# Optimization experiments

Measured on AMD Instinct MI355X. Metric: run time of the kernel, lower is better.

The kernel has to match this reference:

```python
import jax, jax.numpy as jnp
import numpy as np

DECAY = 0.99
EPS = 1e-05


def setup_inputs() -> dict:
    key = jax.random.key(0)
    k1, k2 = jax.random.split(key)
    N, D, K = 262144, 32, 1024
    z = jax.random.normal(k1, (N, D), dtype=jnp.float32)
    # xavier_normal_ on (K, D): std = sqrt(2 / (K + D))
    std = float(np.sqrt(2.0 / (K + D)))
    embedding = jax.random.normal(k2, (K, D), dtype=jnp.float32) * std
    embed_avg = embedding  # buffer initialized as a clone of the codebook
    cluster_size = jnp.ones((K,), dtype=jnp.float32)
    return {"z": z, "embedding": embedding, "embed_avg": embed_avg,
            "cluster_size": cluster_size}


def reference(z, embedding, embed_avg, cluster_size):
    n_embed, embed_dim = embedding.shape
    # squared euclidean cdist: ||z||^2 + ||e||^2 - 2 z e^T  -> [N, K]
    d = (jnp.sum(z * z, axis=1, keepdims=True)
         + jnp.sum(embedding * embedding, axis=1)
         - 2.0 * (z @ embedding.T))
    encoding_indices = jnp.argmin(d, axis=1)  # [N]
    # one-hot column sums via scatter-add (counts per code)
    counts = jnp.zeros((n_embed,), z.dtype).at[encoding_indices].add(1.0)
    unused_codes = jnp.sum(counts == 0)
    # embedding gather
    z_q = embedding[encoding_indices]  # [N, D]
    # EMA scatter-add update (training branch, use_ema=True)
    embed_sum = jnp.zeros_like(embedding).at[encoding_indices].add(z)  # [K, D]
    cluster_size_new = DECAY * cluster_size + (1.0 - DECAY) * counts
    embed_avg_new = DECAY * embed_avg + (1.0 - DECAY) * embed_sum
    n = jnp.sum(cluster_size_new)
    norm_w = n * (cluster_size_new + EPS) / (n + n_embed * EPS)  # Laplace smoothing
    embedding_new = embed_avg_new / norm_w[:, None]
    codebook_loss = jnp.float32(0.0)
    commitment_loss = jnp.mean((z - jax.lax.stop_gradient(z_q)) ** 2)
    # straight-through estimator
    z_q_out = z + jax.lax.stop_gradient(z_q - z)
    return (z_q_out, codebook_loss, commitment_loss, encoding_indices,
            unused_codes, embedding_new, cluster_size_new, embed_avg_new)
```

## Files before the change

kernel.cpp:

```cpp
#include <hip/hip_runtime.h>
#include <hip/hip_bf16.h>
#include <float.h>

#define DIM 32
#define KCODES 1024
#define NROWS 262144

#define O_ZQ   0
#define O_CB   8388608
#define O_CL   8388609
#define O_IDX  8388610
#define O_UN   8650754
#define O_EMB  8650755
#define O_CS   8683523
#define O_EA   8684547

#define W_PCNT 0
#define W_PSUM 262144
#define W_PCOM 8650752
#define W_NORM 8651008
#define W_ZZH  8652032
#define W_EEH  8914176
#define W_BF   8915200

typedef __attribute__((ext_vector_type(8))) short bf16x8;
typedef __attribute__((ext_vector_type(4))) float f32x4;

#define MFMA16 __builtin_amdgcn_mfma_f32_16x16x32_bf16

static __device__ __forceinline__ unsigned short f2bf(float x) {
    __hip_bfloat16 h = __float2bfloat16(x);
    return __builtin_bit_cast(unsigned short, h);
}
static __device__ __forceinline__ float bf2f(unsigned short u) {
    unsigned int v = ((unsigned int)u) << 16;
    return __builtin_bit_cast(float, v);
}
static __device__ __forceinline__ float pw8_sq(const float* x) {
    float w[32];
    #pragma unroll
    for (int i = 0; i < 32; ++i) w[i] = __fmul_rn(x[i], x[i]);
    float r[8];
    #pragma unroll
    for (int j = 0; j < 8; ++j) r[j] = ((w[j] + w[8 + j]) + w[16 + j]) + w[24 + j];
    return ((r[0] + r[1]) + (r[2] + r[3])) + ((r[4] + r[5]) + (r[6] + r[7]));
}

__global__ __launch_bounds__(256) void vq_prep_z(
    const float* __restrict__ z, float* __restrict__ ws)
{
    int row = blockIdx.x * 256 + threadIdx.x;
    float x[32];
    const float4* zg = (const float4*)(z + (size_t)row * DIM);
    #pragma unroll
    for (int q = 0; q < 8; ++q) {
        float4 v = zg[q];
        x[4*q] = v.x; x[4*q+1] = v.y; x[4*q+2] = v.z; x[4*q+3] = v.w;
    }
    ws[W_ZZH + row] = 0.5f * pw8_sq(x);
}

__global__ __launch_bounds__(256) void vq_prep_e(
    const float* __restrict__ emb, float* __restrict__ ws)
{
    int c = blockIdx.x * 256 + threadIdx.x;
    float x[32];
    const float4* eg = (const float4*)(emb + (size_t)c * DIM);
    #pragma unroll
    for (int q = 0; q < 8; ++q) {
        float4 v = eg[q];
        x[4*q] = v.x; x[4*q+1] = v.y; x[4*q+2] = v.z; x[4*q+3] = v.w;
    }
    ws[W_EEH + c] = 0.5f * pw8_sq(x);

    unsigned short hb[3][32];
    #pragma unroll
    for (int i = 0; i < 32; ++i) {
        float v = x[i];
        unsigned short h0 = f2bf(v); float f0 = bf2f(h0); float r1 = v - f0;
        unsigned short h1 = f2bf(r1); float f1 = bf2f(h1); float r2 = r1 - f1;
        unsigned short h2 = f2bf(r2);
        hb[0][i] = h0; hb[1][i] = h1; hb[2][i] = h2;
    }
    bf16x8* bf = (bf16x8*)(ws + W_BF);
    int kt = c >> 4, cl = c & 15;
    #pragma unroll
    for (int s = 0; s < 3; ++s) {
        #pragma unroll
        for (int j = 0; j < 4; ++j) {
            bf16x8 pk;
            #pragma unroll
            for (int e = 0; e < 8; ++e) pk[e] = (short)hb[s][j*8 + e];
            bf[(kt*3 + s)*64 + j*16 + cl] = pk;
        }
    }
}

__global__ __launch_bounds__(256, 4) void vq_argmin_mfma(
    const float* __restrict__ z, const float* __restrict__ wsc,
    float* __restrict__ out)
{
    __shared__ float eesh[1024];
    const int t = threadIdx.x;
    const int lane = t & 63, w = t >> 6;
    const int g = lane >> 4, lr = lane & 15;

    const bf16x8* bvG = (const bf16x8*)(wsc + W_BF);

    #pragma unroll
    for (int i = 0; i < 4; ++i) eesh[t + i * 256] = wsc[W_EEH + t + i * 256];

    const int rtbase = blockIdx.x * 16 + w * 4;
    bf16x8 zh[4], zm[4], zl[4];
    float zza[4][4];
    #pragma unroll
    for (int j = 0; j < 4; ++j) {
        const int rtg = rtbase + j;
        const float* zp = z + ((size_t)(rtg * 16 + lr)) * DIM + g * 8;
        float4 a4 = *(const float4*)zp, b4 = *(const float4*)(zp + 4);
        float xs[8] = {a4.x, a4.y, a4.z, a4.w, b4.x, b4.y, b4.z, b4.w};
        #pragma unroll
        for (int e = 0; e < 8; ++e) {
            float v = xs[e];
            unsigned short h0 = f2bf(v); float f0 = bf2f(h0); float r1 = v - f0;
            unsigned short h1 = f2bf(r1); float f1 = bf2f(h1); float r2 = r1 - f1;
            zh[j][e] = (short)h0; zm[j][e] = (short)h1; zl[j][e] = (short)f2bf(r2);
        }
        float4 zv = *(const float4*)(wsc + W_ZZH + rtg * 16 + g * 4);
        zza[j][0] = zv.x; zza[j][1] = zv.y; zza[j][2] = zv.z; zza[j][3] = zv.w;
    }

    unsigned int Bb[4][4]; int Kk[4][4];
    #pragma unroll
    for (int j = 0; j < 4; ++j)
        #pragma unroll
        for (int r = 0; r < 4; ++r) { Bb[j][r] = 0xFFFFFFFFu; Kk[j][r] = 0; }

    __syncthreads();

    #pragma unroll 2
    for (int kt = 0; kt < 64; ++kt) {
        bf16x8 eh = bvG[(kt * 3 + 0) * 64 + lane];
        bf16x8 em = bvG[(kt * 3 + 1) * 64 + lane];
        bf16x8 el = bvG[(kt * 3 + 2) * 64 + lane];
        float ee_l = eesh[kt * 16 + lr];
        int kge = kt * 16 + lr;
        #pragma unroll
        for (int j = 0; j < 4; ++j) {
            f32x4 a = {0.f, 0.f, 0.f, 0.f};
            a = MFMA16(zh[j], eh, a, 0, 0, 0);
            a = MFMA16(zh[j], em, a, 0, 0, 0);
            a = MFMA16(zm[j], eh, a, 0, 0, 0);
            a = MFMA16(zh[j], el, a, 0, 0, 0);
            a = MFMA16(zl[j], eh, a, 0, 0, 0);
            a = MFMA16(zm[j], em, a, 0, 0, 0);
            #pragma unroll
            for (int r = 0; r < 4; ++r) {
                float v = (zza[j][r] + ee_l) - a[r];
                unsigned int u = __builtin_bit_cast(unsigned int, v);
                bool tk = u < Bb[j][r];
                Bb[j][r] = tk ? u : Bb[j][r];
                Kk[j][r] = tk ? kge : Kk[j][r];
            }
        }
    }

    #pragma unroll
    for (int j = 0; j < 4; ++j) {
        const int rtg = rtbase + j;
        #pragma unroll
        for (int r = 0; r < 4; ++r) {
            unsigned int b0 = Bb[j][r]; int k0 = Kk[j][r];
            #pragma unroll
            for (int m = 1; m < 16; m <<= 1) {
                unsigned int ob = __shfl_xor((int)b0, m, 16); int ok = __shfl_xor(k0, m, 16);
                bool tk = (ob < b0) || (ob == b0 && ok < k0);
                b0 = tk ? ob : b0; k0 = tk ? ok : k0;
            }
            if (lr == 0) out[O_IDX + rtg * 16 + g * 4 + r] = (float)k0;
        }
    }
}

__global__ __launch_bounds__(1024) void vq_scatter(
    const float* __restrict__ z, const float* __restrict__ emb,
    float* __restrict__ out, float* __restrict__ ws)
{
    __shared__ float smem[34816];
    __shared__ float red[16];
    const int t = threadIdx.x;
    const int b = blockIdx.x;
    {
        float4 zero4 = {0.f, 0.f, 0.f, 0.f};
        float4* s4 = (float4*)smem;
        #pragma unroll
        for (int i = 0; i < 9; ++i) { int j = t + i * 1024; if (j < 8704) s4[j] = zero4; }
    }
    __syncthreads();

    const int row = b * 1024 + t;
    const int kk = (int)out[O_IDX + row];
    const float4* zg = (const float4*)(z + (size_t)row * DIM);
    const float4* eg = (const float4*)(emb + (size_t)kk * DIM);
    float4* og = (float4*)(out + O_ZQ + (size_t)row * DIM);
    float zv[32];
    float csum = 0.f;
    #pragma unroll
    for (int q = 0; q < 8; ++q) {
        float4 v = zg[q];
        float4 e = eg[q];
        zv[4*q] = v.x; zv[4*q+1] = v.y; zv[4*q+2] = v.z; zv[4*q+3] = v.w;
        float d0 = v.x - e.x, d1 = v.y - e.y, d2 = v.z - e.z, d3 = v.w - e.w;
        csum = fmaf(d0, d0, csum); csum = fmaf(d1, d1, csum);
        csum = fmaf(d2, d2, csum); csum = fmaf(d3, d3, csum);
        float4 o;
        o.x = v.x + (e.x - v.x); o.y = v.y + (e.y - v.y);
        o.z = v.z + (e.z - v.z); o.w = v.w + (e.w - v.w);
        og[q] = o;
    }
    atomicAdd(&smem[33792 + kk], 1.0f);
    #pragma unroll
    for (int i = 0; i < 32; ++i) atomicAdd(&smem[kk * 33 + i], zv[i]);

    #pragma unroll
    for (int off = 32; off > 0; off >>= 1) csum += __shfl_down(csum, off, 64);
    if ((t & 63) == 0) red[t >> 6] = csum;
    __syncthreads();

    float cpart = smem[33792 + t];
    if (cpart != 0.f) atomicAdd(&ws[W_PCNT + t], cpart);

    float4* p4 = (float4*)(ws + W_PSUM + (size_t)b * (KCODES * DIM));
    #pragma unroll
    for (int c = 0; c < 8; ++c) {
        int j = t + c * 1024;
        int kr = j >> 3, e0 = (j & 7) * 4;
        float4 v;
        v.x = smem[kr * 33 + e0 + 0]; v.y = smem[kr * 33 + e0 + 1];
        v.z = smem[kr * 33 + e0 + 2]; v.w = smem[kr * 33 + e0 + 3];
        p4[j] = v;
    }
    if (t == 0) {
        float s = 0.f;
        #pragma unroll
        for (int i = 0; i < 16; ++i) s += red[i];
        ws[W_PCOM + b] = s;
    }
}

__global__ __launch_bounds__(1024) void vq_epilogue0(
    const float* __restrict__ cs_in, const float* __restrict__ ws,
    float* __restrict__ out, float* __restrict__ wsw)
{
    __shared__ float s1[1024], s2[1024];
    const int k = threadIdx.x;
    float c = ws[W_PCNT + k];
    float csn = 0.99f * cs_in[k] + 0.01f * c;
    out[O_CS + k] = csn;
    s1[k] = csn;
    s2[k] = (c == 0.f) ? 1.f : 0.f;
    __syncthreads();
    for (int s = 512; s > 0; s >>= 1) {
        if (k < s) { s1[k] += s1[k + s]; s2[k] += s2[k + s]; }
        __syncthreads();
    }
    float n = s1[0];
    float unused = s2[0];
    wsw[W_NORM + k] = n * (csn + 1e-5f) / (n + 1024.f * 1e-5f);
    __syncthreads();
    s1[k] = (k < 256) ? ws[W_PCOM + k] : 0.f;
    __syncthreads();
    for (int s = 512; s > 0; s >>= 1) {
        if (k < s) s1[k] += s1[k + s];
        __syncthreads();
    }
    if (k == 0) {
        out[O_CB] = 0.f;
        out[O_CL] = s1[0] / 8388608.f;
        out[O_UN] = unused;
    }
}

__global__ void vq_epilogue1(
    const float* __restrict__ ea, const float* __restrict__ ws,
    float* __restrict__ out)
{
    const int id = blockIdx.x * 128 + threadIdx.x;
    float es = 0.f;
    for (int bb = 0; bb < 256; ++bb) es += ws[W_PSUM + (size_t)bb * (KCODES * DIM) + id];
    float ean = 0.99f * ea[id] + 0.01f * es;
    out[O_EA + id] = ean;
    out[O_EMB + id] = ean / ws[W_NORM + (id >> 5)];
}

extern "C" void kernel_launch(void* const* d_in, const int* in_sizes, int n_in,
                              void* d_out, int out_size, void* d_ws, size_t ws_size,
                              hipStream_t stream)
{
    const float* z   = (const float*)d_in[0];
    const float* emb = (const float*)d_in[1];
    const float* ea  = (const float*)d_in[2];
    const float* cs  = (const float*)d_in[3];
    float* out = (float*)d_out;
    float* ws  = (float*)d_ws;

    hipMemsetAsync(ws + W_PCNT, 0, KCODES * sizeof(float), stream);
    vq_prep_z<<<1024, 256, 0, stream>>>(z, ws);
    vq_prep_e<<<4, 256, 0, stream>>>(emb, ws);
    vq_argmin_mfma<<<1024, 256, 0, stream>>>(z, ws, out);
    vq_scatter<<<256, 1024, 0, stream>>>(z, emb, out, ws);
    vq_epilogue0<<<1, 1024, 0, stream>>>(cs, ws, out, ws);
    vq_epilogue1<<<256, 128, 0, stream>>>(ea, ws, out);
}
```

Before: 176.8 us.

## Fuse z-norm prep and z_q/commitment output into argmin kernel, halve rows per block

Drops the separate z squared-norm prep kernel and instead computes ||z||^2 inside the argmin kernel with cross-lane shuffles. The straight-through z_q write, the embedding gather and the commitment-loss partial sums also move into the argmin kernel, reconstructing z from its three bf16 splits. Each block now handles 2 row tiles per wave instead of 4, so the grid doubles to 2048 blocks, and the 4-blocks-per-CU launch bound is dropped. This removes one launch and one extra pass over z, and shrinks the scatter kernel to just the atomics. In exchange, each loaded codebook tile is reused over fewer rows, and z values rebuilt from the bf16 splits may differ slightly from the original floats.

```diff
diff --git a/kernel.cpp b/kernel.cpp
--- a/kernel.cpp
+++ b/kernel.cpp
@@ -18,10 +18,9 @@
 #define W_PCNT 0
 #define W_PSUM 262144
 #define W_PCOM 8650752
-#define W_NORM 8651008
-#define W_ZZH  8652032
-#define W_EEH  8914176
-#define W_BF   8915200
+#define W_NORM 8652800
+#define W_EEH  8653824
+#define W_BF   8654848
 
 typedef __attribute__((ext_vector_type(8))) short bf16x8;
 typedef __attribute__((ext_vector_type(4))) float f32x4;
@@ -44,20 +43,6 @@
     #pragma unroll
     for (int j = 0; j < 8; ++j) r[j] = ((w[j] + w[8 + j]) + w[16 + j]) + w[24 + j];
     return ((r[0] + r[1]) + (r[2] + r[3])) + ((r[4] + r[5]) + (r[6] + r[7]));
-}
-
-__global__ __launch_bounds__(256) void vq_prep_z(
-    const float* __restrict__ z, float* __restrict__ ws)
-{
-    int row = blockIdx.x * 256 + threadIdx.x;
-    float x[32];
-    const float4* zg = (const float4*)(z + (size_t)row * DIM);
-    #pragma unroll
-    for (int q = 0; q < 8; ++q) {
-        float4 v = zg[q];
-        x[4*q] = v.x; x[4*q+1] = v.y; x[4*q+2] = v.z; x[4*q+3] = v.w;
-    }
-    ws[W_ZZH + row] = 0.5f * pw8_sq(x);
 }
 
 __global__ __launch_bounds__(256) void vq_prep_e(
@@ -96,11 +81,12 @@
     }
 }
 
-__global__ __launch_bounds__(256, 4) void vq_argmin_mfma(
-    const float* __restrict__ z, const float* __restrict__ wsc,
-    float* __restrict__ out)
+__global__ __launch_bounds__(256) void vq_argmin_mfma(
+    const float* __restrict__ z, const float* __restrict__ emb,
+    const float* __restrict__ wsc, float* __restrict__ out, float* __restrict__ ws)
 {
     __shared__ float eesh[1024];
+    __shared__ float red[4];
     const int t = threadIdx.x;
     const int lane = t & 63, w = t >> 6;
     const int g = lane >> 4, lr = lane & 15;
@@ -110,29 +96,40 @@
     #pragma unroll
     for (int i = 0; i < 4; ++i) eesh[t + i * 256] = wsc[W_EEH + t + i * 256];
 
-    const int rtbase = blockIdx.x * 16 + w * 4;
-    bf16x8 zh[4], zm[4], zl[4];
-    float zza[4][4];
-    #pragma unroll
-    for (int j = 0; j < 4; ++j) {
+    const int rtbase = blockIdx.x * 8 + w * 2;
+    bf16x8 zh[2], zm[2], zl[2];
+    float zza[2][4];
+    #pragma unroll
+    for (int j = 0; j < 2; ++j) {
         const int rtg = rtbase + j;
         const float* zp = z + ((size_t)(rtg * 16 + lr)) * DIM + g * 8;
         float4 a4 = *(const float4*)zp, b4 = *(const float4*)(zp + 4);
         float xs[8] = {a4.x, a4.y, a4.z, a4.w, b4.x, b4.y, b4.z, b4.w};
+        float r8[8];
         #pragma unroll
         for (int e = 0; e < 8; ++e) {
             float v = xs[e];
             unsigned short h0 = f2bf(v); float f0 = bf2f(h0); float r1 = v - f0;
             unsigned short h1 = f2bf(r1); float f1 = bf2f(h1); float r2 = r1 - f1;
             zh[j][e] = (short)h0; zm[j][e] = (short)h1; zl[j][e] = (short)f2bf(r2);
-        }
-        float4 zv = *(const float4*)(wsc + W_ZZH + rtg * 16 + g * 4);
-        zza[j][0] = zv.x; zza[j][1] = zv.y; zza[j][2] = zv.z; zza[j][3] = zv.w;
-    }
-
-    unsigned int Bb[4][4]; int Kk[4][4];
-    #pragma unroll
-    for (int j = 0; j < 4; ++j)
+            float wq = __fmul_rn(v, v);
+            float b16 = __shfl_xor(wq, 16);
+            float b32 = __shfl_xor(wq, 32);
+            float b48 = __shfl_xor(wq, 48);
+            float t1 = (g < 2) ? (wq + b16) : (b32 + b48);
+            float c2 = (g == 0) ? b32 : (g == 1) ? b48 : (g == 2) ? wq : b16;
+            float c3 = (g == 0) ? b48 : (g == 1) ? b32 : (g == 2) ? b16 : wq;
+            r8[e] = (t1 + c2) + c3;
+        }
+        float zzf = ((r8[0] + r8[1]) + (r8[2] + r8[3])) + ((r8[4] + r8[5]) + (r8[6] + r8[7]));
+        float zzh2 = 0.5f * zzf;
+        #pragma unroll
+        for (int r = 0; r < 4; ++r) zza[j][r] = __shfl(zzh2, g * 4 + r, 16);
+    }
+
+    unsigned int Bb[2][4]; int Kk[2][4];
+    #pragma unroll
+    for (int j = 0; j < 2; ++j)
         #pragma unroll
         for (int r = 0; r < 4; ++r) { Bb[j][r] = 0xFFFFFFFFu; Kk[j][r] = 0; }
 
@@ -146,7 +143,7 @@
         float ee_l = eesh[kt * 16 + lr];
         int kge = kt * 16 + lr;
         #pragma unroll
-        for (int j = 0; j < 4; ++j) {
+        for (int j = 0; j < 2; ++j) {
             f32x4 a = {0.f, 0.f, 0.f, 0.f};
             a = MFMA16(zh[j], eh, a, 0, 0, 0);
             a = MFMA16(zh[j], em, a, 0, 0, 0);
@@ -165,9 +162,11 @@
         }
     }
 
-    #pragma unroll
-    for (int j = 0; j < 4; ++j) {
+    float csum = 0.f;
+    #pragma unroll
+    for (int j = 0; j < 2; ++j) {
         const int rtg = rtbase + j;
+        int kfin[4];
         #pragma unroll
         for (int r = 0; r < 4; ++r) {
             unsigned int b0 = Bb[j][r]; int k0 = Kk[j][r];
@@ -177,17 +176,44 @@
                 bool tk = (ob < b0) || (ob == b0 && ok < k0);
                 b0 = tk ? ob : b0; k0 = tk ? ok : k0;
             }
+            kfin[r] = k0;
             if (lr == 0) out[O_IDX + rtg * 16 + g * 4 + r] = (float)k0;
         }
-    }
+        int src = (lr >> 2) * 16;
+        int kr0 = __shfl(kfin[0], src);
+        int kr1 = __shfl(kfin[1], src);
+        int kr2 = __shfl(kfin[2], src);
+        int kr3 = __shfl(kfin[3], src);
+        int sel = lr & 3;
+        int kk = (sel == 0) ? kr0 : (sel == 1) ? kr1 : (sel == 2) ? kr2 : kr3;
+        const float4* ep = (const float4*)(emb + (size_t)kk * DIM + g * 8);
+        float4 e0 = ep[0], e1 = ep[1];
+        float ev[8] = {e0.x, e0.y, e0.z, e0.w, e1.x, e1.y, e1.z, e1.w};
+        float ov[8];
+        #pragma unroll
+        for (int e = 0; e < 8; ++e) {
+            float zv = (bf2f((unsigned short)zh[j][e]) + bf2f((unsigned short)zm[j][e]))
+                     + bf2f((unsigned short)zl[j][e]);
+            float d = zv - ev[e];
+            csum = fmaf(d, d, csum);
+            ov[e] = zv + (ev[e] - zv);
+        }
+        float4* og = (float4*)(out + O_ZQ + (size_t)(rtg * 16 + lr) * DIM + g * 8);
+        og[0] = (float4){ov[0], ov[1], ov[2], ov[3]};
+        og[1] = (float4){ov[4], ov[5], ov[6], ov[7]};
+    }
+    #pragma unroll
+    for (int off = 32; off > 0; off >>= 1) csum += __shfl_down(csum, off, 64);
+    if (lane == 0) red[w] = csum;
+    __syncthreads();
+    if (t == 0) ws[W_PCOM + blockIdx.x] = ((red[0] + red[1]) + (red[2] + red[3]));
 }
 
 __global__ __launch_bounds__(1024) void vq_scatter(
-    const float* __restrict__ z, const float* __restrict__ emb,
-    float* __restrict__ out, float* __restrict__ ws)
+    const float* __restrict__ z, const float* __restrict__ outv,
+    float* __restrict__ ws)
 {
     __shared__ float smem[34816];
-    __shared__ float red[16];
     const int t = threadIdx.x;
     const int b = blockIdx.x;
     {
@@ -199,32 +225,17 @@
     __syncthreads();
 
     const int row = b * 1024 + t;
-    const int kk = (int)out[O_IDX + row];
+    const int kk = (int)outv[O_IDX + row];
     const float4* zg = (const float4*)(z + (size_t)row * DIM);
-    const float4* eg = (const float4*)(emb + (size_t)kk * DIM);
-    float4* og = (float4*)(out + O_ZQ + (size_t)row * DIM);
-    float zv[32];
-    float csum = 0.f;
+    atomicAdd(&smem[33792 + kk], 1.0f);
     #pragma unroll
     for (int q = 0; q < 8; ++q) {
         float4 v = zg[q];
-        float4 e = eg[q];
-        zv[4*q] = v.x; zv[4*q+1] = v.y; zv[4*q+2] = v.z; zv[4*q+3] = v.w;
-        float d0 = v.x - e.x, d1 = v.y - e.y, d2 = v.z - e.z, d3 = v.w - e.w;
-        csum = fmaf(d0, d0, csum); csum = fmaf(d1, d1, csum);
-        csum = fmaf(d2, d2, csum); csum = fmaf(d3, d3, csum);
-        float4 o;
-        o.x = v.x + (e.x - v.x); o.y = v.y + (e.y - v.y);
-        o.z = v.z + (e.z - v.z); o.w = v.w + (e.w - v.w);
-        og[q] = o;
-    }
-    atomicAdd(&smem[33792 + kk], 1.0f);
-    #pragma unroll
-    for (int i = 0; i < 32; ++i) atomicAdd(&smem[kk * 33 + i], zv[i]);
-
-    #pragma unroll
-    for (int off = 32; off > 0; off >>= 1) csum += __shfl_down(csum, off, 64);
-    if ((t & 63) == 0) red[t >> 6] = csum;
+        atomicAdd(&smem[kk * 33 + 4 * q + 0], v.x);
+        atomicAdd(&smem[kk * 33 + 4 * q + 1], v.y);
+        atomicAdd(&smem[kk * 33 + 4 * q + 2], v.z);
+        atomicAdd(&smem[kk * 33 + 4 * q + 3], v.w);
+    }
     __syncthreads();
 
     float cpart = smem[33792 + t];
@@ -240,12 +251,6 @@
         v.z = smem[kr * 33 + e0 + 2]; v.w = smem[kr * 33 + e0 + 3];
         p4[j] = v;
     }
-    if (t == 0) {
-        float s = 0.f;
-        #pragma unroll
-        for (int i = 0; i < 16; ++i) s += red[i];
-        ws[W_PCOM + b] = s;
-    }
 }
 
 __global__ __launch_bounds__(1024) void vq_epilogue0(
@@ -268,7 +273,7 @@
     float unused = s2[0];
     wsw[W_NORM + k] = n * (csn + 1e-5f) / (n + 1024.f * 1e-5f);
     __syncthreads();
-    s1[k] = (k < 256) ? ws[W_PCOM + k] : 0.f;
+    s1[k] = ws[W_PCOM + k] + ws[W_PCOM + 1024 + k];
     __syncthreads();
     for (int s = 512; s > 0; s >>= 1) {
         if (k < s) s1[k] += s1[k + s];
@@ -305,10 +310,9 @@
     float* ws  = (float*)d_ws;
 
     hipMemsetAsync(ws + W_PCNT, 0, KCODES * sizeof(float), stream);
-    vq_prep_z<<<1024, 256, 0, stream>>>(z, ws);
     vq_prep_e<<<4, 256, 0, stream>>>(emb, ws);
-    vq_argmin_mfma<<<1024, 256, 0, stream>>>(z, ws, out);
-    vq_scatter<<<256, 1024, 0, stream>>>(z, emb, out, ws);
+    vq_argmin_mfma<<<2048, 256, 0, stream>>>(z, emb, ws, out, ws);
+    vq_scatter<<<256, 1024, 0, stream>>>(z, out, ws);
     vq_epilogue0<<<1, 1024, 0, stream>>>(cs, ws, out, ws);
     vq_epilogue1<<<256, 128, 0, stream>>>(ea, ws, out);
 }
```

New measurement: 187.3 us. +5.9%, slower.

## Fuse row-norm computation into argmin kernel and halve scatter block count

Applied to the files above, without the earlier changes.

Removes the separate vq_prep_z kernel and computes each row's half squared norm inside the MFMA argmin kernel, combining per-lane partial products with cross-lane shuffles in the same summation order as before. The scatter kernel now handles two rows per thread with 128 blocks instead of 256. That halves the per-block partial-sum buffers that the epilogue has to reduce and cuts the number of partial commitment sums. The aim is to save one kernel launch and one pass over z, plus epilogue reduction traffic, at the cost of lower parallelism in the scatter kernel and extra shuffles in argmin.

```diff
diff --git a/kernel.cpp b/kernel.cpp
--- a/kernel.cpp
+++ b/kernel.cpp
@@ -18,10 +18,9 @@
 #define W_PCNT 0
 #define W_PSUM 262144
 #define W_PCOM 8650752
-#define W_NORM 8651008
-#define W_ZZH  8652032
-#define W_EEH  8914176
-#define W_BF   8915200
+#define W_NORM 8652800
+#define W_EEH  8653824
+#define W_BF   8654848
 
 typedef __attribute__((ext_vector_type(8))) short bf16x8;
 typedef __attribute__((ext_vector_type(4))) float f32x4;
@@ -44,20 +43,6 @@
     #pragma unroll
     for (int j = 0; j < 8; ++j) r[j] = ((w[j] + w[8 + j]) + w[16 + j]) + w[24 + j];
     return ((r[0] + r[1]) + (r[2] + r[3])) + ((r[4] + r[5]) + (r[6] + r[7]));
-}
-
-__global__ __launch_bounds__(256) void vq_prep_z(
-    const float* __restrict__ z, float* __restrict__ ws)
-{
-    int row = blockIdx.x * 256 + threadIdx.x;
-    float x[32];
-    const float4* zg = (const float4*)(z + (size_t)row * DIM);
-    #pragma unroll
-    for (int q = 0; q < 8; ++q) {
-        float4 v = zg[q];
-        x[4*q] = v.x; x[4*q+1] = v.y; x[4*q+2] = v.z; x[4*q+3] = v.w;
-    }
-    ws[W_ZZH + row] = 0.5f * pw8_sq(x);
 }
 
 __global__ __launch_bounds__(256) void vq_prep_e(
@@ -119,15 +104,26 @@
         const float* zp = z + ((size_t)(rtg * 16 + lr)) * DIM + g * 8;
         float4 a4 = *(const float4*)zp, b4 = *(const float4*)(zp + 4);
         float xs[8] = {a4.x, a4.y, a4.z, a4.w, b4.x, b4.y, b4.z, b4.w};
+        float r8[8];
         #pragma unroll
         for (int e = 0; e < 8; ++e) {
             float v = xs[e];
             unsigned short h0 = f2bf(v); float f0 = bf2f(h0); float r1 = v - f0;
             unsigned short h1 = f2bf(r1); float f1 = bf2f(h1); float r2 = r1 - f1;
             zh[j][e] = (short)h0; zm[j][e] = (short)h1; zl[j][e] = (short)f2bf(r2);
-        }
-        float4 zv = *(const float4*)(wsc + W_ZZH + rtg * 16 + g * 4);
-        zza[j][0] = zv.x; zza[j][1] = zv.y; zza[j][2] = zv.z; zza[j][3] = zv.w;
+            float wq = __fmul_rn(v, v);
+            float b16 = __shfl_xor(wq, 16);
+            float b32 = __shfl_xor(wq, 32);
+            float b48 = __shfl_xor(wq, 48);
+            float t1 = (g < 2) ? (wq + b16) : (b32 + b48);
+            float c2 = (g == 0) ? b32 : (g == 1) ? b48 : (g == 2) ? wq : b16;
+            float c3 = (g == 0) ? b48 : (g == 1) ? b32 : (g == 2) ? b16 : wq;
+            r8[e] = (t1 + c2) + c3;
+        }
+        float zzf = ((r8[0] + r8[1]) + (r8[2] + r8[3])) + ((r8[4] + r8[5]) + (r8[6] + r8[7]));
+        float zzh2 = 0.5f * zzf;
+        #pragma unroll
+        for (int r = 0; r < 4; ++r) zza[j][r] = __shfl(zzh2, g * 4 + r, 16);
     }
 
     unsigned int Bb[4][4]; int Kk[4][4];
@@ -198,29 +194,32 @@
     }
     __syncthreads();
 
-    const int row = b * 1024 + t;
-    const int kk = (int)out[O_IDX + row];
-    const float4* zg = (const float4*)(z + (size_t)row * DIM);
-    const float4* eg = (const float4*)(emb + (size_t)kk * DIM);
-    float4* og = (float4*)(out + O_ZQ + (size_t)row * DIM);
-    float zv[32];
     float csum = 0.f;
     #pragma unroll
-    for (int q = 0; q < 8; ++q) {
-        float4 v = zg[q];
-        float4 e = eg[q];
-        zv[4*q] = v.x; zv[4*q+1] = v.y; zv[4*q+2] = v.z; zv[4*q+3] = v.w;
-        float d0 = v.x - e.x, d1 = v.y - e.y, d2 = v.z - e.z, d3 = v.w - e.w;
-        csum = fmaf(d0, d0, csum); csum = fmaf(d1, d1, csum);
-        csum = fmaf(d2, d2, csum); csum = fmaf(d3, d3, csum);
-        float4 o;
-        o.x = v.x + (e.x - v.x); o.y = v.y + (e.y - v.y);
-        o.z = v.z + (e.z - v.z); o.w = v.w + (e.w - v.w);
-        og[q] = o;
-    }
-    atomicAdd(&smem[33792 + kk], 1.0f);
-    #pragma unroll
-    for (int i = 0; i < 32; ++i) atomicAdd(&smem[kk * 33 + i], zv[i]);
+    for (int rr = 0; rr < 2; ++rr) {
+        const int row = b * 2048 + rr * 1024 + t;
+        const int kk = (int)out[O_IDX + row];
+        const float4* zg = (const float4*)(z + (size_t)row * DIM);
+        const float4* eg = (const float4*)(emb + (size_t)kk * DIM);
+        float4* og = (float4*)(out + O_ZQ + (size_t)row * DIM);
+        atomicAdd(&smem[33792 + kk], 1.0f);
+        #pragma unroll
+        for (int q = 0; q < 8; ++q) {
+            float4 v = zg[q];
+            float4 e = eg[q];
+            float d0 = v.x - e.x, d1 = v.y - e.y, d2 = v.z - e.z, d3 = v.w - e.w;
+            csum = fmaf(d0, d0, csum); csum = fmaf(d1, d1, csum);
+            csum = fmaf(d2, d2, csum); csum = fmaf(d3, d3, csum);
+            float4 o;
+            o.x = v.x + (e.x - v.x); o.y = v.y + (e.y - v.y);
+            o.z = v.z + (e.z - v.z); o.w = v.w + (e.w - v.w);
+            og[q] = o;
+            atomicAdd(&smem[kk * 33 + 4 * q + 0], v.x);
+            atomicAdd(&smem[kk * 33 + 4 * q + 1], v.y);
+            atomicAdd(&smem[kk * 33 + 4 * q + 2], v.z);
+            atomicAdd(&smem[kk * 33 + 4 * q + 3], v.w);
+        }
+    }
 
     #pragma unroll
     for (int off = 32; off > 0; off >>= 1) csum += __shfl_down(csum, off, 64);
@@ -268,7 +267,7 @@
     float unused = s2[0];
     wsw[W_NORM + k] = n * (csn + 1e-5f) / (n + 1024.f * 1e-5f);
     __syncthreads();
-    s1[k] = (k < 256) ? ws[W_PCOM + k] : 0.f;
+    s1[k] = (k < 128) ? ws[W_PCOM + k] : 0.f;
     __syncthreads();
     for (int s = 512; s > 0; s >>= 1) {
         if (k < s) s1[k] += s1[k + s];
@@ -287,7 +286,7 @@
 {
     const int id = blockIdx.x * 128 + threadIdx.x;
     float es = 0.f;
-    for (int bb = 0; bb < 256; ++bb) es += ws[W_PSUM + (size_t)bb * (KCODES * DIM) + id];
+    for (int bb = 0; bb < 128; ++bb) es += ws[W_PSUM + (size_t)bb * (KCODES * DIM) + id];
     float ean = 0.99f * ea[id] + 0.01f * es;
     out[O_EA + id] = ean;
     out[O_EMB + id] = ean / ws[W_NORM + (id >> 5)];
@@ -305,10 +304,9 @@
     float* ws  = (float*)d_ws;
 
     hipMemsetAsync(ws + W_PCNT, 0, KCODES * sizeof(float), stream);
-    vq_prep_z<<<1024, 256, 0, stream>>>(z, ws);
     vq_prep_e<<<4, 256, 0, stream>>>(emb, ws);
     vq_argmin_mfma<<<1024, 256, 0, stream>>>(z, ws, out);
-    vq_scatter<<<256, 1024, 0, stream>>>(z, emb, out, ws);
+    vq_scatter<<<128, 1024, 0, stream>>>(z, emb, out, ws);
     vq_epilogue0<<<1, 1024, 0, stream>>>(cs, ws, out, ws);
     vq_epilogue1<<<256, 128, 0, stream>>>(ea, ws, out);
 }
```

Result: slower. 205.5 us (+16.2%).
